# Kernel optimization log

Measured on AMD Instinct MI355X. Metric: run time of the kernel, lower is better.

Reference implementation:

```python
import jax, jax.numpy as jnp
import numpy as np

B, T, D = 1, 4096, 2048
H, HKV = 16, 4
DH = D // H            # 128
GROUP = H // HKV       # 4
ROPE_BASE = 10000.0


def setup_inputs() -> dict:
    key = jax.random.key(0)
    kx, kq, kk, kv, ko = jax.random.split(key, 5)
    s = 0.02
    return {
        "x": jax.random.normal(kx, (B, T, D), dtype=jnp.float32),
        "Wq": jax.random.normal(kq, (D, D), dtype=jnp.float32) * s,
        "Wk": jax.random.normal(kk, (D, HKV * DH), dtype=jnp.float32) * s,
        "Wv": jax.random.normal(kv, (D, HKV * DH), dtype=jnp.float32) * s,
        "Wo": jax.random.normal(ko, (D, D), dtype=jnp.float32) * s,
    }


def _rope_sincos(t, half):
    inv_freq = 1.0 / (ROPE_BASE ** (jnp.arange(half, dtype=jnp.float32) / half))
    ang = jnp.arange(t, dtype=jnp.float32)[:, None] * inv_freq  # [T, half]
    # broadcast over batch and head dims: [1, T, 1, half]
    return jnp.sin(ang)[None, :, None, :], jnp.cos(ang)[None, :, None, :]


def _apply_rope(x, sin, cos, half):
    x1, x2 = x[..., :half], x[..., half:]
    return jnp.concatenate([x1 * cos - x2 * sin, x1 * sin + x2 * cos], axis=-1)


def reference(x, Wq, Wk, Wv, Wo):
    b, t, d = x.shape
    q = (x @ Wq).reshape(b, t, H, DH)      # [B,T,H,Dh], H ordered (Hkv, group)
    k = (x @ Wk).reshape(b, t, HKV, DH)    # [B,T,Hkv,Dh]
    v = (x @ Wv).reshape(b, t, HKV, DH)

    half = DH // 2
    sin, cos = _rope_sincos(t, half)
    q = _apply_rope(q, sin, cos, half)
    k = _apply_rope(k, sin, cos, half)

    # GQA without materializing repeated K/V: split q heads into (kv_head, group)
    qg = q.reshape(b, t, HKV, GROUP, DH)
    att = jnp.einsum('bthgd,bshd->bhgts', qg, k) / np.float32(np.sqrt(DH))
    causal = jnp.tril(jnp.ones((t, t), dtype=bool))
    att = jnp.where(causal[None, None, None, :, :], att, -jnp.inf)
    att = jax.nn.softmax(att, axis=-1)
    y = jnp.einsum('bhgts,bshd->bthgd', att, v).reshape(b, t, d)
    return y @ Wo
```

## Files before the change

kernel.cpp:

```cpp
#include <hip/hip_runtime.h>
#include <hip/hip_bf16.h>

#define TT 4096
#define DD 2048
#define NH 16
#define NKV 4
#define DHD 128
#define NQKV 3072

typedef __attribute__((ext_vector_type(8))) short short8;
typedef __attribute__((ext_vector_type(4))) float f32x4;
typedef __hip_bfloat16 bf16;

#define GLOAD_LDS16(g, l)                                                \
    __builtin_amdgcn_global_load_lds(                                    \
        (const __attribute__((address_space(1))) unsigned int*)(g),      \
        (__attribute__((address_space(3))) unsigned int*)(l), 16, 0, 0)

__global__ void cast_x_kernel(const float* __restrict__ x, bf16* __restrict__ xb, int n) {
    int i = (blockIdx.x * blockDim.x + threadIdx.x) * 4;
    if (i >= n) return;
    float4 v = *(const float4*)(x + i);
    xb[i + 0] = __float2bfloat16(v.x);
    xb[i + 1] = __float2bfloat16(v.y);
    xb[i + 2] = __float2bfloat16(v.z);
    xb[i + 3] = __float2bfloat16(v.w);
}

__global__ void transpose_cast_all(const float* __restrict__ Wq, const float* __restrict__ Wk,
                                   const float* __restrict__ Wv, const float* __restrict__ Wo,
                                   bf16* __restrict__ Wt, bf16* __restrict__ Wot) {
    __shared__ float tile[32][33];
    const float* in;
    bf16* out;
    int N, rowOff;
    switch (blockIdx.z) {
        case 0: in = Wq; out = Wt; N = 2048; rowOff = 0; break;
        case 1: in = Wk; out = Wt; N = 512; rowOff = 2048; break;
        case 2: in = Wv; out = Wt; N = 512; rowOff = 2560; break;
        default: in = Wo; out = Wot; N = 2048; rowOff = 0; break;
    }
    int n0 = blockIdx.y * 32;
    if (n0 >= N) return;
    int k0 = blockIdx.x * 32;
    int tx = threadIdx.x, ty = threadIdx.y;
#pragma unroll
    for (int i = 0; i < 4; ++i)
        tile[ty + i * 8][tx] = in[(size_t)(k0 + ty + i * 8) * N + n0 + tx];
    __syncthreads();
#pragma unroll
    for (int i = 0; i < 4; ++i)
        out[(size_t)(rowOff + n0 + ty + i * 8) * 2048 + k0 + tx] = __float2bfloat16(tile[tx][ty + i * 8]);
}

template <bool OUT_BF16>
__global__ __launch_bounds__(256) void gemm_bt_kernel(const bf16* __restrict__ A,
                                                      const bf16* __restrict__ Bt,
                                                      void* __restrict__ C,
                                                      int M, int N, int K) {
    __shared__ bf16 As[128 * 32];
    __shared__ bf16 Bs[128 * 32];
    int nwg = gridDim.x * gridDim.y;
    int orig = blockIdx.y * gridDim.x + blockIdx.x;
    int swz = (orig & 7) * (nwg >> 3) + (orig >> 3);
    int bx = swz % gridDim.x, by = swz / gridDim.x;
    int bn0 = bx * 128, bm0 = by * 128;
    int tid = threadIdx.x;
    int wave = tid >> 6, lane = tid & 63, quad = lane >> 4, l15 = lane & 15;
    int wm = (wave >> 1) * 64, wn = (wave & 1) * 64;

    int srow = wave * 32 + (lane >> 2);
    int scol = (lane & 3) * 8;
    const bf16* gA = A + (size_t)(bm0 + srow) * K + scol;
    const bf16* gB = Bt + (size_t)(bn0 + srow) * K + scol;
    bf16* lA = As + srow * 32 + scol;
    bf16* lB = Bs + srow * 32 + scol;

    f32x4 zero = {0.f, 0.f, 0.f, 0.f};
    f32x4 acc[4][4];
#pragma unroll
    for (int i = 0; i < 4; ++i)
#pragma unroll
        for (int j = 0; j < 4; ++j) acc[i][j] = zero;

    for (int k0 = 0; k0 < K; k0 += 32) {
        GLOAD_LDS16(gA + k0, lA);
        GLOAD_LDS16(gA + k0 + (size_t)16 * K, lA + 16 * 32);
        GLOAD_LDS16(gB + k0, lB);
        GLOAD_LDS16(gB + k0 + (size_t)16 * K, lB + 16 * 32);
        __syncthreads();
        short8 af[4], bfr[4];
#pragma unroll
        for (int i = 0; i < 4; ++i) af[i] = *(const short8*)&As[(wm + i * 16 + l15) * 32 + quad * 8];
#pragma unroll
        for (int j = 0; j < 4; ++j) bfr[j] = *(const short8*)&Bs[(wn + j * 16 + l15) * 32 + quad * 8];
#pragma unroll
        for (int i = 0; i < 4; ++i)
#pragma unroll
            for (int j = 0; j < 4; ++j)
                acc[i][j] = __builtin_amdgcn_mfma_f32_16x16x32_bf16(af[i], bfr[j], acc[i][j], 0, 0, 0);
        __syncthreads();
    }
#pragma unroll
    for (int i = 0; i < 4; ++i)
#pragma unroll
        for (int j = 0; j < 4; ++j)
#pragma unroll
            for (int r = 0; r < 4; ++r) {
                int row = bm0 + wm + i * 16 + quad * 4 + r;
                int col = bn0 + wn + j * 16 + l15;
                float v = acc[i][j][r];
                if (OUT_BF16)
                    ((bf16*)C)[(size_t)row * N + col] = __float2bfloat16(v);
                else
                    ((float*)C)[(size_t)row * N + col] = v;
            }
}

__global__ void rope_split_kernel(const bf16* __restrict__ QKV, bf16* __restrict__ Qs,
                                  bf16* __restrict__ Ks, bf16* __restrict__ Vr) {
    int slot = blockIdx.x * 4 + (threadIdx.x >> 6);
    int d = threadIdx.x & 63;
    int t = slot / 24, c = slot % 24;
    const bf16* base = QKV + (size_t)t * NQKV;
    int off = (c < 16) ? c * 128 : (c < 20) ? 2048 + (c - 16) * 128 : 2560 + (c - 20) * 128;
    float x1 = __bfloat162float(base[off + d]);
    float x2 = __bfloat162float(base[off + 64 + d]);
    float o1, o2;
    if (c < 20) {
        float invf = __expf((float)d * -0.14391156831f);
        float ang = (float)t * invf;
        float sn = sinf(ang), cs = cosf(ang);
        o1 = x1 * cs - x2 * sn;
        o2 = x1 * sn + x2 * cs;
    } else {
        o1 = x1;
        o2 = x2;
    }
    if (c < 16) {
        const float scale = 0.12751741f;
        o1 *= scale;
        o2 *= scale;
        bf16* dst = Qs + ((size_t)c * TT + t) * DHD;
        dst[d] = __float2bfloat16(o1);
        dst[d + 64] = __float2bfloat16(o2);
    } else if (c < 20) {
        bf16* dst = Ks + ((size_t)(c - 16) * TT + t) * DHD;
        dst[d] = __float2bfloat16(o1);
        dst[d + 64] = __float2bfloat16(o2);
    } else {
        int gg = c - 20;
        bf16* dst = Vr + ((size_t)gg * TT + t) * DHD;
        dst[d] = __float2bfloat16(o1);
        dst[d + 64] = __float2bfloat16(o2);
    }
}

__global__ void transpose_v_kernel(const bf16* __restrict__ Vr, bf16* __restrict__ Vt) {
    __shared__ short tile[64][80];
    int g = blockIdx.z;
    int t0 = blockIdx.x * 64, d0 = blockIdx.y * 64;
    int tid = threadIdx.x;
#pragma unroll
    for (int i = 0; i < 2; ++i) {
        int lin = i * 2048 + tid * 8;
        int r = lin >> 6, c = lin & 63;
        *(short8*)&tile[r][c] = *(const short8*)(Vr + ((size_t)g * TT + t0 + r) * DHD + d0 + c);
    }
    __syncthreads();
#pragma unroll
    for (int i = 0; i < 2; ++i) {
        int lin = i * 2048 + tid * 8;
        int r = lin >> 6, c = lin & 63;
        short8 v;
#pragma unroll
        for (int j = 0; j < 8; ++j) v[j] = tile[c + j][r];
        *(short8*)(Vt + ((size_t)g * DHD + d0 + r) * TT + t0 + c) = v;
    }
}

__global__ __launch_bounds__(512, 4) void attn_kernel(const bf16* __restrict__ Qs,
                                                      const bf16* __restrict__ Ks,
                                                      const bf16* __restrict__ Vt,
                                                      bf16* __restrict__ Y) {
    __shared__ __attribute__((aligned(16))) char smem[78848];
    int h = blockIdx.y, bpair = blockIdx.x, g = h >> 2;
    int tid = threadIdx.x, wave = tid >> 6, lane = tid & 63, quad = lane >> 4, l15 = lane & 15;
    int grp = wave >> 2;
    int w = wave & 3;
    int gtid = tid & 255;

    char* Kbase = smem + grp * 34816;
    bf16* PsW = (bf16*)(smem + 69632 + wave * 1024);
    float* Obuf = (float*)(smem + 16384);
    float* mlbuf = (float*)(smem + 77824);

    const bf16* kg = Ks + (size_t)g * TT * DHD;
    const bf16* vg = Vt + (size_t)g * DHD * TT;
    f32x4 zero = {0.f, 0.f, 0.f, 0.f};

    int kOff[2], vOff[2], lOff[2];
#pragma unroll
    for (int r = 0; r < 2; ++r) {
        int idx = r * 256 + gtid;
        int krow = idx >> 4;
        kOff[r] = krow * DHD + ((idx & 15) ^ (krow & 15)) * 8;
        int vrow = idx >> 2;
        vOff[r] = vrow * TT + ((idx & 3) ^ ((vrow >> 1) & 3)) * 8;
        lOff[r] = idx * 8;
    }
    int fsw = (l15 >> 1) & 3;

    for (int pass = 0; pass < 2; ++pass) {
        int qt = (pass == 0) ? bpair : 63 - bpair;
        int qbase = qt * 64 + w * 16;

        if (tid < 256) {
            int g2 = tid >> 7, b2 = (tid >> 6) & 1, e0 = (tid & 63) * 8;
            short fill = (e0 < 32) ? (short)0x3F80 : (short)0;
            short8 v8 = {fill, fill, fill, fill, fill, fill, fill, fill};
            *(short8*)((bf16*)(smem + g2 * 34816 + 16384 + b2 * 9216) + 4096 + e0) = v8;
        }

        short8 qf[4];
        const bf16* qptr = Qs + ((size_t)h * TT + qbase + l15) * DHD + quad * 8;
#pragma unroll
        for (int ks = 0; ks < 4; ++ks) qf[ks] = *(const short8*)(qptr + ks * 32);

        f32x4 acc[9];
#pragma unroll
        for (int i = 0; i < 9; ++i) acc[i] = zero;
        float m_i = -1e30f;

        const bf16* kS = kg + (size_t)(grp * 32) * DHD;
        const bf16* vS = vg + grp * 32;
        int nIter = qt + 1;

#pragma unroll
        for (int r = 0; r < 2; ++r) {
            GLOAD_LDS16(kS + kOff[r], (bf16*)Kbase + lOff[r]);
            GLOAD_LDS16(vS + vOff[r], (bf16*)(Kbase + 16384) + lOff[r]);
        }
        __syncthreads();

        int jb = 0;
        for (int j = 0; j < nIter; ++j) {
            int kt = 2 * j + grp;
            if (j + 1 < nIter) {
#pragma unroll
                for (int r = 0; r < 2; ++r) {
                    GLOAD_LDS16(kS + 64 * DHD + kOff[r], (bf16*)(Kbase + (jb ? 0 : 8192)) + lOff[r]);
                    GLOAD_LDS16(vS + 64 + vOff[r], (bf16*)(Kbase + 16384 + (jb ? 0 : 9216)) + lOff[r]);
                }
            }
            const bf16* Kl = (const bf16*)(Kbase + (jb ? 8192 : 0));
            const bf16* Vl = (const bf16*)(Kbase + 16384 + (jb ? 9216 : 0));
            int dbase = 2 * kt - 4 * qt - w;
            if (dbase <= 0) {
                f32x4 s[2];
                __builtin_amdgcn_s_setprio(1);
#pragma unroll
                for (int nt = 0; nt < 2; ++nt) {
                    int dnt = dbase + nt;
                    if (dnt <= 0) {
                        s[nt] = zero;
#pragma unroll
                        for (int ks = 0; ks < 4; ++ks) {
                            int ch = (ks * 4 + quad) ^ l15;
                            short8 kf = *(const short8*)&Kl[(nt * 16 + l15) * 128 + ch * 8];
                            s[nt] = __builtin_amdgcn_mfma_f32_16x16x32_bf16(kf, qf[ks], s[nt], 0, 0, 0);
                        }
                        if (dnt == 0) {
#pragma unroll
                            for (int r = 0; r < 4; ++r)
                                if (quad * 4 + r > l15) s[nt][r] = -1e30f;
                        }
                    } else {
#pragma unroll
                        for (int r = 0; r < 4; ++r) s[nt][r] = -1e30f;
                    }
                }
                __builtin_amdgcn_s_setprio(0);

                float mloc = fmaxf(fmaxf(s[0][0], s[0][1]), fmaxf(s[0][2], s[0][3]));
                mloc = fmaxf(mloc, fmaxf(fmaxf(s[1][0], s[1][1]), fmaxf(s[1][2], s[1][3])));
                mloc = fmaxf(mloc, __shfl_xor(mloc, 16));
                mloc = fmaxf(mloc, __shfl_xor(mloc, 32));
                if (__any(mloc > m_i + 8.0f)) {
                    float mnew = fmaxf(m_i, mloc);
                    float alpha = exp2f(m_i - mnew);
                    m_i = mnew;
#pragma unroll
                    for (int d8 = 0; d8 < 9; ++d8)
#pragma unroll
                        for (int r = 0; r < 4; ++r) acc[d8][r] *= alpha;
                }
#pragma unroll
                for (int nt = 0; nt < 2; ++nt)
#pragma unroll
                    for (int r = 0; r < 4; ++r) s[nt][r] = exp2f(s[nt][r] - m_i);

#pragma unroll
                for (int nt = 0; nt < 2; ++nt)
#pragma unroll
                    for (int rr = 0; rr < 2; ++rr) {
                        int col = nt * 16 + quad * 4 + rr * 2;
                        int ch = (col >> 3) ^ fsw;
                        __hip_bfloat162 pk;
                        pk.x = __float2bfloat16(s[nt][rr * 2]);
                        pk.y = __float2bfloat16(s[nt][rr * 2 + 1]);
                        *(__hip_bfloat162*)&PsW[l15 * 32 + ch * 8 + (col & 7)] = pk;
                    }
                asm volatile("s_waitcnt lgkmcnt(0)" ::: "memory");

                int chp = quad ^ fsw;
                short8 pf = *(const short8*)&PsW[l15 * 32 + chp * 8];
                __builtin_amdgcn_s_setprio(1);
#pragma unroll
                for (int d8 = 0; d8 < 9; ++d8) {
                    short8 vf = *(const short8*)&Vl[(d8 * 16 + l15) * 32 + chp * 8];
                    acc[d8] = __builtin_amdgcn_mfma_f32_16x16x32_bf16(vf, pf, acc[d8], 0, 0, 0);
                }
                __builtin_amdgcn_s_setprio(0);
            }
            __syncthreads();
            jb ^= 1;
            kS += 64 * DHD;
            vS += 64;
        }

        if (quad == 0) {
            mlbuf[(wave * 16 + l15) * 2] = m_i;
            mlbuf[(wave * 16 + l15) * 2 + 1] = acc[8][0];
        }
        __syncthreads();
        if (grp == 1) {
            float m_a = mlbuf[(w * 16 + l15) * 2];
            float mm = fmaxf(m_a, m_i);
            float fb = exp2f(m_i - mm);
            float* ob = Obuf + (w * 16 + l15) * 132;
#pragma unroll
            for (int d8 = 0; d8 < 8; ++d8) {
                f32x4 t = acc[d8] * fb;
                *(f32x4*)&ob[d8 * 16 + quad * 4] = t;
            }
        }
        __syncthreads();
        if (grp == 0) {
            float m_b = mlbuf[((w + 4) * 16 + l15) * 2];
            float l_b = mlbuf[((w + 4) * 16 + l15) * 2 + 1];
            float l_a = mlbuf[(w * 16 + l15) * 2 + 1];
            float mm = fmaxf(m_i, m_b);
            float fa = exp2f(m_i - mm);
            float fb = exp2f(m_b - mm);
            float lt = l_a * fa + l_b * fb;
            float* ob = Obuf + (w * 16 + l15) * 132;
#pragma unroll
            for (int d8 = 0; d8 < 8; ++d8) {
                f32x4 t = *(const f32x4*)&ob[d8 * 16 + quad * 4];
                acc[d8] = acc[d8] * fa + t;
            }
            float linv = 1.0f / lt;

            bf16* ow = (bf16*)smem + w * 2048;
#pragma unroll
            for (int d8 = 0; d8 < 8; ++d8)
#pragma unroll
                for (int rr = 0; rr < 2; ++rr) {
                    int colD = d8 * 16 + quad * 4 + rr * 2;
                    int ch = (colD >> 3) ^ (l15 & 7);
                    __hip_bfloat162 o2;
                    o2.x = __float2bfloat16(acc[d8][rr * 2] * linv);
                    o2.y = __float2bfloat16(acc[d8][rr * 2 + 1] * linv);
                    *(__hip_bfloat162*)&ow[l15 * 128 + ch * 8 + (colD & 7)] = o2;
                }
            asm volatile("s_waitcnt lgkmcnt(0)" ::: "memory");
#pragma unroll
            for (int c = 0; c < 4; ++c) {
                int chunk = quad * 4 + c;
                int ch = chunk ^ (l15 & 7);
                short8 ov = *(const short8*)&ow[l15 * 128 + ch * 8];
                *(short8*)&Y[(size_t)(qbase + l15) * DD + h * DHD + chunk * 8] = ov;
            }
        }
        __syncthreads();
    }
}

extern "C" void kernel_launch(void* const* d_in, const int* in_sizes, int n_in,
                              void* d_out, int out_size, void* d_ws, size_t ws_size,
                              hipStream_t stream) {
    const float* x = (const float*)d_in[0];
    const float* Wq = (const float*)d_in[1];
    const float* Wk = (const float*)d_in[2];
    const float* Wv = (const float*)d_in[3];
    const float* Wo = (const float*)d_in[4];

    char* ws = (char*)d_ws;
    size_t off = 0;
    auto alloc = [&](size_t bytes) {
        void* p = ws + off;
        off += (bytes + 255) & ~(size_t)255;
        return p;
    };
    bf16* xb = (bf16*)alloc((size_t)TT * DD * 2);
    bf16* Wt = (bf16*)alloc((size_t)NQKV * DD * 2);
    bf16* Wot = (bf16*)alloc((size_t)DD * DD * 2);
    bf16* QKVb = (bf16*)alloc((size_t)TT * NQKV * 2);
    bf16* Qs = (bf16*)alloc((size_t)NH * TT * DHD * 2);
    bf16* Ksb = (bf16*)alloc((size_t)NKV * TT * DHD * 2);
    bf16* Vrb = (bf16*)alloc((size_t)NKV * TT * DHD * 2);
    bf16* Vtb = (bf16*)alloc((size_t)NKV * DHD * TT * 2);
    bf16* Yb = (bf16*)alloc((size_t)TT * DD * 2);

    cast_x_kernel<<<(TT * DD / 4 + 255) / 256, 256, 0, stream>>>(x, xb, TT * DD);
    transpose_cast_all<<<dim3(64, 64, 4), dim3(32, 8), 0, stream>>>(Wq, Wk, Wv, Wo, Wt, Wot);

    gemm_bt_kernel<true><<<dim3(NQKV / 128, TT / 128), 256, 0, stream>>>(xb, Wt, QKVb, TT, NQKV, DD);
    rope_split_kernel<<<TT * 24 / 4, 256, 0, stream>>>(QKVb, Qs, Ksb, Vrb);
    transpose_v_kernel<<<dim3(TT / 64, DHD / 64, NKV), 256, 0, stream>>>(Vrb, Vtb);
    attn_kernel<<<dim3(32, NH), 512, 0, stream>>>(Qs, Ksb, Vtb, Yb);
    gemm_bt_kernel<false><<<dim3(DD / 128, TT / 128), 256, 0, stream>>>(Yb, Wot, d_out, TT, DD, DD);
}
```

Measured before the change: 396.9 us.

## Replace GEMM with 256-row tiles, 4-stage LDS pipeline and swizzled LDS layout

Replaces the single-buffered 128x128 GEMM with a 512-thread kernel using 256xBN tiles, a 4-slot global->LDS prefetch ring gated by explicit vmcnt waits, and an XOR swizzle on LDS columns to reduce bank conflicts. It also raises MFMA priority around the compute loop. The aim is to hide global load latency and increase data reuse per tile in both the QKV and output projections. In exchange it uses more LDS and registers, which may lower occupancy, and it depends on hand-tuned waitcnt counts for correctness.

New measurement: 410.5 us. 3.4% more time.

```diff
diff --git a/kernel.cpp b/kernel.cpp
--- a/kernel.cpp
+++ b/kernel.cpp
@@ -53,58 +53,100 @@
         out[(size_t)(rowOff + n0 + ty + i * 8) * 2048 + k0 + tx] = __float2bfloat16(tile[tx][ty + i * 8]);
 }
 
-template <bool OUT_BF16>
-__global__ __launch_bounds__(256) void gemm_bt_kernel(const bf16* __restrict__ A,
-                                                      const bf16* __restrict__ Bt,
-                                                      void* __restrict__ C,
-                                                      int M, int N, int K) {
-    __shared__ bf16 As[128 * 32];
-    __shared__ bf16 Bs[128 * 32];
+template <int BN, bool OUT_BF16>
+__global__ __launch_bounds__(512, 2) void gemm256_kernel(const bf16* __restrict__ A,
+                                                         const bf16* __restrict__ Bt,
+                                                         void* __restrict__ C,
+                                                         int M, int N, int K) {
+    constexpr int NJ = BN / 64;
+    constexpr int NLB = BN / 128;
+    constexpr int ASLOT = 256 * 32;
+    constexpr int BSLOT = BN * 32;
+    __shared__ __attribute__((aligned(16))) bf16 As[4 * ASLOT];
+    __shared__ __attribute__((aligned(16))) bf16 Bs[4 * BSLOT];
+
     int nwg = gridDim.x * gridDim.y;
     int orig = blockIdx.y * gridDim.x + blockIdx.x;
     int swz = (orig & 7) * (nwg >> 3) + (orig >> 3);
     int bx = swz % gridDim.x, by = swz / gridDim.x;
-    int bn0 = bx * 128, bm0 = by * 128;
+    int bn0 = bx * BN, bm0 = by * 256;
+
     int tid = threadIdx.x;
     int wave = tid >> 6, lane = tid & 63, quad = lane >> 4, l15 = lane & 15;
-    int wm = (wave >> 1) * 64, wn = (wave & 1) * 64;
-
-    int srow = wave * 32 + (lane >> 2);
-    int scol = (lane & 3) * 8;
-    const bf16* gA = A + (size_t)(bm0 + srow) * K + scol;
-    const bf16* gB = Bt + (size_t)(bn0 + srow) * K + scol;
-    bf16* lA = As + srow * 32 + scol;
-    bf16* lB = Bs + srow * 32 + scol;
+    int wm = (wave >> 2) * 128, wn = (wave & 3) * (BN / 4);
+    int fsw = (l15 >> 1) & 3;
+
+    size_t aoff[2];
+    int ldsA[2];
+#pragma unroll
+    for (int ld = 0; ld < 2; ++ld) {
+        int idx = ld * 512 + tid;
+        int row = idx >> 2, c = idx & 3;
+        aoff[ld] = (size_t)(bm0 + row) * K + ((c ^ ((row >> 1) & 3)) * 8);
+        ldsA[ld] = idx * 8;
+    }
+    size_t boff[NLB];
+    int ldsB[NLB];
+#pragma unroll
+    for (int ld = 0; ld < NLB; ++ld) {
+        int idx = ld * 512 + tid;
+        int row = idx >> 2, c = idx & 3;
+        boff[ld] = (size_t)(bn0 + row) * K + ((c ^ ((row >> 1) & 3)) * 8);
+        ldsB[ld] = idx * 8;
+    }
+
+    auto STAGE = [&](int t, int s) {
+        const bf16* a = A + (size_t)t * 32;
+        const bf16* b = Bt + (size_t)t * 32;
+#pragma unroll
+        for (int ld = 0; ld < 2; ++ld) GLOAD_LDS16(a + aoff[ld], &As[s * ASLOT + ldsA[ld]]);
+#pragma unroll
+        for (int ld = 0; ld < NLB; ++ld) GLOAD_LDS16(b + boff[ld], &Bs[s * BSLOT + ldsB[ld]]);
+    };
 
     f32x4 zero = {0.f, 0.f, 0.f, 0.f};
-    f32x4 acc[4][4];
-#pragma unroll
-    for (int i = 0; i < 4; ++i)
-#pragma unroll
-        for (int j = 0; j < 4; ++j) acc[i][j] = zero;
-
-    for (int k0 = 0; k0 < K; k0 += 32) {
-        GLOAD_LDS16(gA + k0, lA);
-        GLOAD_LDS16(gA + k0 + (size_t)16 * K, lA + 16 * 32);
-        GLOAD_LDS16(gB + k0, lB);
-        GLOAD_LDS16(gB + k0 + (size_t)16 * K, lB + 16 * 32);
-        __syncthreads();
-        short8 af[4], bfr[4];
-#pragma unroll
-        for (int i = 0; i < 4; ++i) af[i] = *(const short8*)&As[(wm + i * 16 + l15) * 32 + quad * 8];
-#pragma unroll
-        for (int j = 0; j < 4; ++j) bfr[j] = *(const short8*)&Bs[(wn + j * 16 + l15) * 32 + quad * 8];
-#pragma unroll
-        for (int i = 0; i < 4; ++i)
-#pragma unroll
-            for (int j = 0; j < 4; ++j)
+    f32x4 acc[8][NJ];
+#pragma unroll
+    for (int i = 0; i < 8; ++i)
+#pragma unroll
+        for (int j = 0; j < NJ; ++j) acc[i][j] = zero;
+
+    int NT = K >> 5;
+    STAGE(0, 0);
+    STAGE(1, 1);
+    STAGE(2, 2);
+
+    for (int kt = 0; kt < NT; ++kt) {
+        int pf = kt + 3;
+        if (pf > NT - 1) pf = NT - 1;
+        STAGE(pf, (kt + 3) & 3);
+        if constexpr (BN == 256)
+            asm volatile("s_waitcnt vmcnt(12)\n\ts_barrier" ::: "memory");
+        else
+            asm volatile("s_waitcnt vmcnt(9)\n\ts_barrier" ::: "memory");
+        const bf16* as = &As[(kt & 3) * ASLOT];
+        const bf16* bs = &Bs[(kt & 3) * BSLOT];
+        short8 af[8], bfr[NJ];
+#pragma unroll
+        for (int i = 0; i < 8; ++i)
+            af[i] = *(const short8*)&as[(wm + i * 16 + l15) * 32 + (quad ^ fsw) * 8];
+#pragma unroll
+        for (int j = 0; j < NJ; ++j)
+            bfr[j] = *(const short8*)&bs[(wn + j * 16 + l15) * 32 + (quad ^ fsw) * 8];
+        __builtin_amdgcn_s_setprio(1);
+#pragma unroll
+        for (int i = 0; i < 8; ++i)
+#pragma unroll
+            for (int j = 0; j < NJ; ++j)
                 acc[i][j] = __builtin_amdgcn_mfma_f32_16x16x32_bf16(af[i], bfr[j], acc[i][j], 0, 0, 0);
-        __syncthreads();
-    }
-#pragma unroll
-    for (int i = 0; i < 4; ++i)
-#pragma unroll
-        for (int j = 0; j < 4; ++j)
+        __builtin_amdgcn_s_setprio(0);
+        asm volatile("s_waitcnt lgkmcnt(0)\n\ts_barrier" ::: "memory");
+    }
+
+#pragma unroll
+    for (int i = 0; i < 8; ++i)
+#pragma unroll
+        for (int j = 0; j < NJ; ++j)
 #pragma unroll
             for (int r = 0; r < 4; ++r) {
                 int row = bm0 + wm + i * 16 + quad * 4 + r;
@@ -416,9 +458,9 @@
     cast_x_kernel<<<(TT * DD / 4 + 255) / 256, 256, 0, stream>>>(x, xb, TT * DD);
     transpose_cast_all<<<dim3(64, 64, 4), dim3(32, 8), 0, stream>>>(Wq, Wk, Wv, Wo, Wt, Wot);
 
-    gemm_bt_kernel<true><<<dim3(NQKV / 128, TT / 128), 256, 0, stream>>>(xb, Wt, QKVb, TT, NQKV, DD);
+    gemm256_kernel<256, true><<<dim3(NQKV / 256, TT / 256), 512, 0, stream>>>(xb, Wt, QKVb, TT, NQKV, DD);
     rope_split_kernel<<<TT * 24 / 4, 256, 0, stream>>>(QKVb, Qs, Ksb, Vrb);
     transpose_v_kernel<<<dim3(TT / 64, DHD / 64, NKV), 256, 0, stream>>>(Vrb, Vtb);
     attn_kernel<<<dim3(32, NH), 512, 0, stream>>>(Qs, Ksb, Vtb, Yb);
-    gemm_bt_kernel<false><<<dim3(DD / 128, TT / 128), 256, 0, stream>>>(Yb, Wot, d_out, TT, DD, DD);
-}
+    gemm256_kernel<128, false><<<dim3(DD / 128, TT / 256), 512, 0, stream>>>(Yb, Wot, d_out, TT, DD, DD);
+}
```

## Double GEMM K-tile depth and read V directly from QKV in transpose

Applied to the files above, without the earlier changes.

The GEMM kernel now stages a 64-wide K slice per iteration instead of 32 and runs two MFMA sub-steps per barrier pair, halving the number of syncthreads and loop overhead. Separately, the rope kernel no longer copies V into an intermediate buffer; the V transpose kernel reads V straight from the fused QKV output. This trades doubled LDS use per GEMM block (possibly lower occupancy) for fewer barriers and one fewer global round trip for V.

Result: slower. 421.1 us (+6.1%).

```diff
diff --git a/kernel.cpp b/kernel.cpp
--- a/kernel.cpp
+++ b/kernel.cpp
@@ -58,8 +58,8 @@
                                                       const bf16* __restrict__ Bt,
                                                       void* __restrict__ C,
                                                       int M, int N, int K) {
-    __shared__ bf16 As[128 * 32];
-    __shared__ bf16 Bs[128 * 32];
+    __shared__ bf16 As[128 * 64];
+    __shared__ bf16 Bs[128 * 64];
     int nwg = gridDim.x * gridDim.y;
     int orig = blockIdx.y * gridDim.x + blockIdx.x;
     int swz = (orig & 7) * (nwg >> 3) + (orig >> 3);
@@ -69,12 +69,13 @@
     int wave = tid >> 6, lane = tid & 63, quad = lane >> 4, l15 = lane & 15;
     int wm = (wave >> 1) * 64, wn = (wave & 1) * 64;
 
-    int srow = wave * 32 + (lane >> 2);
-    int scol = (lane & 3) * 8;
-    const bf16* gA = A + (size_t)(bm0 + srow) * K + scol;
-    const bf16* gB = Bt + (size_t)(bn0 + srow) * K + scol;
-    bf16* lA = As + srow * 32 + scol;
-    bf16* lB = Bs + srow * 32 + scol;
+    int sRow[4], sCol[4];
+#pragma unroll
+    for (int r = 0; r < 4; ++r) {
+        int idx = r * 256 + tid;
+        sRow[r] = idx >> 3;
+        sCol[r] = (idx & 7) * 8;
+    }
 
     f32x4 zero = {0.f, 0.f, 0.f, 0.f};
     f32x4 acc[4][4];
@@ -83,22 +84,28 @@
 #pragma unroll
         for (int j = 0; j < 4; ++j) acc[i][j] = zero;
 
-    for (int k0 = 0; k0 < K; k0 += 32) {
-        GLOAD_LDS16(gA + k0, lA);
-        GLOAD_LDS16(gA + k0 + (size_t)16 * K, lA + 16 * 32);
-        GLOAD_LDS16(gB + k0, lB);
-        GLOAD_LDS16(gB + k0 + (size_t)16 * K, lB + 16 * 32);
-        __syncthreads();
-        short8 af[4], bfr[4];
-#pragma unroll
-        for (int i = 0; i < 4; ++i) af[i] = *(const short8*)&As[(wm + i * 16 + l15) * 32 + quad * 8];
-#pragma unroll
-        for (int j = 0; j < 4; ++j) bfr[j] = *(const short8*)&Bs[(wn + j * 16 + l15) * 32 + quad * 8];
-#pragma unroll
-        for (int i = 0; i < 4; ++i)
+    for (int k0 = 0; k0 < K; k0 += 64) {
+#pragma unroll
+        for (int r = 0; r < 4; ++r) {
+            GLOAD_LDS16(A + (size_t)(bm0 + sRow[r]) * K + k0 + sCol[r], As + (r * 256 + tid) * 8);
+            GLOAD_LDS16(Bt + (size_t)(bn0 + sRow[r]) * K + k0 + sCol[r], Bs + (r * 256 + tid) * 8);
+        }
+        __syncthreads();
+#pragma unroll
+        for (int s = 0; s < 2; ++s) {
+            short8 af[4], bfr[4];
+#pragma unroll
+            for (int i = 0; i < 4; ++i)
+                af[i] = *(const short8*)&As[(wm + i * 16 + l15) * 64 + s * 32 + quad * 8];
 #pragma unroll
             for (int j = 0; j < 4; ++j)
-                acc[i][j] = __builtin_amdgcn_mfma_f32_16x16x32_bf16(af[i], bfr[j], acc[i][j], 0, 0, 0);
+                bfr[j] = *(const short8*)&Bs[(wn + j * 16 + l15) * 64 + s * 32 + quad * 8];
+#pragma unroll
+            for (int i = 0; i < 4; ++i)
+#pragma unroll
+                for (int j = 0; j < 4; ++j)
+                    acc[i][j] = __builtin_amdgcn_mfma_f32_16x16x32_bf16(af[i], bfr[j], acc[i][j], 0, 0, 0);
+        }
         __syncthreads();
     }
 #pragma unroll
@@ -118,25 +125,19 @@
 }
 
 __global__ void rope_split_kernel(const bf16* __restrict__ QKV, bf16* __restrict__ Qs,
-                                  bf16* __restrict__ Ks, bf16* __restrict__ Vr) {
+                                  bf16* __restrict__ Ks) {
     int slot = blockIdx.x * 4 + (threadIdx.x >> 6);
     int d = threadIdx.x & 63;
-    int t = slot / 24, c = slot % 24;
+    int t = slot / 20, c = slot % 20;
     const bf16* base = QKV + (size_t)t * NQKV;
-    int off = (c < 16) ? c * 128 : (c < 20) ? 2048 + (c - 16) * 128 : 2560 + (c - 20) * 128;
+    int off = (c < 16) ? c * 128 : 2048 + (c - 16) * 128;
     float x1 = __bfloat162float(base[off + d]);
     float x2 = __bfloat162float(base[off + 64 + d]);
-    float o1, o2;
-    if (c < 20) {
-        float invf = __expf((float)d * -0.14391156831f);
-        float ang = (float)t * invf;
-        float sn = sinf(ang), cs = cosf(ang);
-        o1 = x1 * cs - x2 * sn;
-        o2 = x1 * sn + x2 * cs;
-    } else {
-        o1 = x1;
-        o2 = x2;
-    }
+    float invf = __expf((float)d * -0.14391156831f);
+    float ang = (float)t * invf;
+    float sn = sinf(ang), cs = cosf(ang);
+    float o1 = x1 * cs - x2 * sn;
+    float o2 = x1 * sn + x2 * cs;
     if (c < 16) {
         const float scale = 0.12751741f;
         o1 *= scale;
@@ -144,19 +145,14 @@
         bf16* dst = Qs + ((size_t)c * TT + t) * DHD;
         dst[d] = __float2bfloat16(o1);
         dst[d + 64] = __float2bfloat16(o2);
-    } else if (c < 20) {
+    } else {
         bf16* dst = Ks + ((size_t)(c - 16) * TT + t) * DHD;
         dst[d] = __float2bfloat16(o1);
         dst[d + 64] = __float2bfloat16(o2);
-    } else {
-        int gg = c - 20;
-        bf16* dst = Vr + ((size_t)gg * TT + t) * DHD;
-        dst[d] = __float2bfloat16(o1);
-        dst[d + 64] = __float2bfloat16(o2);
-    }
-}
-
-__global__ void transpose_v_kernel(const bf16* __restrict__ Vr, bf16* __restrict__ Vt) {
+    }
+}
+
+__global__ void transpose_v_kernel(const bf16* __restrict__ QKV, bf16* __restrict__ Vt) {
     __shared__ short tile[64][80];
     int g = blockIdx.z;
     int t0 = blockIdx.x * 64, d0 = blockIdx.y * 64;
@@ -165,7 +161,8 @@
     for (int i = 0; i < 2; ++i) {
         int lin = i * 2048 + tid * 8;
         int r = lin >> 6, c = lin & 63;
-        *(short8*)&tile[r][c] = *(const short8*)(Vr + ((size_t)g * TT + t0 + r) * DHD + d0 + c);
+        *(short8*)&tile[r][c] =
+            *(const short8*)(QKV + (size_t)(t0 + r) * NQKV + 2560 + g * 128 + d0 + c);
     }
     __syncthreads();
 #pragma unroll
@@ -409,7 +406,6 @@
     bf16* QKVb = (bf16*)alloc((size_t)TT * NQKV * 2);
     bf16* Qs = (bf16*)alloc((size_t)NH * TT * DHD * 2);
     bf16* Ksb = (bf16*)alloc((size_t)NKV * TT * DHD * 2);
-    bf16* Vrb = (bf16*)alloc((size_t)NKV * TT * DHD * 2);
     bf16* Vtb = (bf16*)alloc((size_t)NKV * DHD * TT * 2);
     bf16* Yb = (bf16*)alloc((size_t)TT * DD * 2);
 
@@ -417,8 +413,8 @@
     transpose_cast_all<<<dim3(64, 64, 4), dim3(32, 8), 0, stream>>>(Wq, Wk, Wv, Wo, Wt, Wot);
 
     gemm_bt_kernel<true><<<dim3(NQKV / 128, TT / 128), 256, 0, stream>>>(xb, Wt, QKVb, TT, NQKV, DD);
-    rope_split_kernel<<<TT * 24 / 4, 256, 0, stream>>>(QKVb, Qs, Ksb, Vrb);
-    transpose_v_kernel<<<dim3(TT / 64, DHD / 64, NKV), 256, 0, stream>>>(Vrb, Vtb);
+    rope_split_kernel<<<TT * 20 / 4, 256, 0, stream>>>(QKVb, Qs, Ksb);
+    transpose_v_kernel<<<dim3(TT / 64, DHD / 64, NKV), 256, 0, stream>>>(QKVb, Vtb);
     attn_kernel<<<dim3(32, NH), 512, 0, stream>>>(Qs, Ksb, Vtb, Yb);
     gemm_bt_kernel<false><<<dim3(DD / 128, TT / 128), 256, 0, stream>>>(Yb, Wot, d_out, TT, DD, DD);
 }
```
